# Optimization experiments

Measured on AMD Instinct MI355X. Metric: run time of the kernel, lower is better.

## Reference

```python
import jax, jax.numpy as jnp
import numpy as np

V, D, B, NEG = 100000, 128, 4096, 5
D_INNER = int(D * 2.0 * 2 / 3)  # nGPT FF inner dim = 170

def l2norm(t, axis=-1):
    return t / jnp.linalg.norm(t, axis=axis, keepdims=True)

def setup_inputs() -> dict:
    key = jax.random.key(0)
    ks = jax.random.split(key, 8)
    return {
        "input_ids": jax.random.randint(ks[0], (B,), 0, V),
        "target_ids": jax.random.randint(ks[1], (B,), 0, V),
        "neg_ids": jax.random.randint(ks[2], (B, NEG), 0, V),
        "W_in": jax.random.normal(ks[3], (V, D), jnp.float32) * (1.0 / np.sqrt(D)),
        "W_out": jax.random.normal(ks[4], (V, D), jnp.float32) * (1.0 / np.sqrt(D)),
        "W_hidden": jax.random.normal(ks[5], (D_INNER, D), jnp.float32) * 0.02,
        "W_gate": jax.random.normal(ks[6], (D_INNER, D), jnp.float32) * 0.02,
        "W_ff_out": jax.random.normal(ks[7], (D, D_INNER), jnp.float32) * 0.02,
        "hidden_scale": jnp.ones((D_INNER,), jnp.float32),
        "gate_scale": jnp.ones((D_INNER,), jnp.float32),
        "logit_scale": jnp.full((V,), D ** -0.5, dtype=jnp.float32),  # Scale param init = s_logit_scale
    }

def reference(input_ids, target_ids, neg_ids, W_in, W_out, W_hidden, W_gate,
              W_ff_out, hidden_scale, gate_scale, logit_scale):
    # skipgram: gather normalized input embeddings
    emb = l2norm(W_in)[input_ids]                                  # (B, D)
    # nGPT FeedForward: silu-gated, weights l2-normalized on input dim
    h = (emb @ l2norm(W_hidden).T) * hidden_scale                  # (B, D_INNER)
    g = (emb @ l2norm(W_gate).T) * gate_scale * jnp.sqrt(jnp.float32(D))
    x = jax.nn.silu(g) * h
    x = x @ l2norm(W_ff_out, axis=0).T                             # (B, D), to_out norm_dim_in=False
    # logits over full vocab, scaled by Scale(): param * (init/scale)
    scale_eff = logit_scale * (1.0 / (D ** -0.5))                  # (V,)
    logits = (x @ l2norm(W_out).T) * scale_eff                     # (B, V)
    # negative-sampling loss: gather positive + sampled negative logits
    pos = jnp.take_along_axis(logits, target_ids[:, None], axis=1)  # (B, 1)
    neg = jnp.take_along_axis(logits, neg_ids, axis=1)              # (B, NEG)
    positive_loss = jax.nn.log_sigmoid(pos).mean()
    negative_loss = jax.nn.log_sigmoid(-neg).mean()
    return -(positive_loss + negative_loss)
```

## Files before the change

kernel.cpp:

```cpp
#include <hip/hip_runtime.h>
#include <math.h>

#define DD    128
#define DI    170
#define DIP   176
#define ND4   32
#define ND4H  16
#define NI4P  44
#define BB    4096
#define NNEG  5
#define ROWS  8
#define NBLK  (BB / ROWS)
#define NTHR  512
#define NTASK (ROWS * (1 + NNEG))
#define XOP   132
#define SQRT_D 11.3137084989847603904f

#define WS_WHT 0
#define WS_WGT (ND4 * DIP * 4)
#define WS_WFT (2 * ND4 * DIP * 4)

#define GLOAD_LDS4(gptr, lptr)                                                  \
    __builtin_amdgcn_global_load_lds(                                           \
        (const __attribute__((address_space(1))) void*)(gptr),                  \
        (__attribute__((address_space(3))) void*)(lptr), 4, 0, 0)

#define BAR_LGKM() asm volatile("s_waitcnt lgkmcnt(0)\n\ts_barrier" ::: "memory")

__device__ __forceinline__ float wave_bcast_sum(float v) {
#pragma unroll
    for (int m = 1; m < 64; m <<= 1) v += __shfl_xor(v, m, 64);
    return v;
}

__global__ __launch_bounds__(256) void prep_kernel(
    const float* __restrict__ W_hidden,
    const float* __restrict__ W_gate,
    const float* __restrict__ W_ff_out,
    const float* __restrict__ hidden_scale,
    const float* __restrict__ gate_scale,
    float* __restrict__ ws,
    float* __restrict__ out)
{
    if (blockIdx.x == 0 && threadIdx.x == 0) out[0] = 0.0f;
    const int wave = threadIdx.x >> 6;
    const int lane = threadIdx.x & 63;
    const int t = blockIdx.x * 4 + wave;
    float* whT = ws + WS_WHT;
    float* wgT = ws + WS_WGT;
    float* wfT = ws + WS_WFT;

    if (t < DI) {
        const int v = t;
        float a = W_ff_out[(long)(2 * lane)     * DI + v];
        float b = W_ff_out[(long)(2 * lane + 1) * DI + v];
        float cf = wave_bcast_sum(a * a + b * b);
        float2 ph = ((const float2*)(W_hidden + (long)v * DD))[lane];
        float2 pg = ((const float2*)(W_gate   + (long)v * DD))[lane];
        float sh = wave_bcast_sum(ph.x * ph.x + ph.y * ph.y);
        float sg = wave_bcast_sum(pg.x * pg.x + pg.y * pg.y);
        const float whs = rsqrtf(sh) * hidden_scale[v] * rsqrtf(cf);
        const float wgs = rsqrtf(sg) * gate_scale[v] * SQRT_D;
        const int d4   = lane >> 1;
        const int half = lane & 1;
        float2* dh = (float2*)(whT + ((long)d4 * DIP + v) * 4 + half * 2);
        *dh = make_float2(ph.x * whs, ph.y * whs);
        float2* dg = (float2*)(wgT + ((long)d4 * DIP + v) * 4 + half * 2);
        *dg = make_float2(pg.x * wgs, pg.y * wgs);
    } else if (t < DI + NI4P) {
        const int i4 = t - DI;
#pragma unroll
        for (int rr = 0; rr < 2; ++rr) {
            const int dd = rr * 64 + lane;
            float4 v4;
            if (i4 < 42) {
                float2 lo = *(const float2*)(W_ff_out + (long)dd * DI + 4 * i4);
                float2 hi = *(const float2*)(W_ff_out + (long)dd * DI + 4 * i4 + 2);
                v4 = make_float4(lo.x, lo.y, hi.x, hi.y);
            } else if (i4 == 42) {
                float2 lo = *(const float2*)(W_ff_out + (long)dd * DI + 168);
                v4 = make_float4(lo.x, lo.y, 0.0f, 0.0f);
            } else {
                v4 = make_float4(0.0f, 0.0f, 0.0f, 0.0f);
            }
            *(float4*)(wfT + ((long)i4 * DD + dd) * 4) = v4;
        }
    } else if (t == DI + NI4P || t == DI + NI4P + 1) {
        float* base = (t == DI + NI4P) ? whT : wgT;
        for (int idx = lane; idx < ND4 * 6; idx += 64) {
            const int d4 = idx / 6, c = idx % 6;
            *(float4*)(base + ((long)d4 * DIP + DI + c) * 4) =
                make_float4(0.0f, 0.0f, 0.0f, 0.0f);
        }
    }
}

__global__ __launch_bounds__(NTHR, 4) void main_kernel(
    const int*   __restrict__ input_ids,
    const int*   __restrict__ target_ids,
    const int*   __restrict__ neg_ids,
    const float* __restrict__ W_in,
    const float* __restrict__ W_out,
    const float* __restrict__ logit_scale,
    const float* __restrict__ ws,
    float* __restrict__ out)
{
    __shared__ __align__(16) float s_emb[ROWS][DD];
    __shared__ __align__(16) float s_x[ROWS][DIP];
    __shared__ __align__(16) float s_pp[4][ROWS][DD];
    __shared__ __align__(16) float s_xout[ROWS][XOP];
    __shared__ __align__(16) float s_wout[NTASK][DD];
    __shared__ float s_part[DIP][2 * ROWS + 1];
    __shared__ float s_dp[NTASK][9];
    __shared__ float s_sp[NTASK][9];
    __shared__ float s_psc[NTASK];
    __shared__ float s_ls[NTASK];

    const int tid  = threadIdx.x;
    const int wave = tid >> 6;
    const int lane = tid & 63;
    const int b0   = blockIdx.x * ROWS;

    const float4* whT4 = (const float4*)(ws + WS_WHT);
    const float4* wgT4 = (const float4*)(ws + WS_WGT);
    const float4* wfT4 = (const float4*)(ws + WS_WFT);

    {
        const int id = input_ids[b0 + wave];
        float2 p = ((const float2*)(W_in + (long)id * DD))[lane];
        float s  = wave_bcast_sum(p.x * p.x + p.y * p.y);
        float inv = rsqrtf(s);
        s_emb[wave][2 * lane]     = p.x * inv;
        s_emb[wave][2 * lane + 1] = p.y * inv;
    }
    BAR_LGKM();

    const bool gA = (tid < DIP);
    const bool gB = (tid >= 256 && tid < 256 + DIP);
    const int i = gA ? tid : (gB ? tid - 256 : -1);
    float ah[ROWS], ag[ROWS];
#pragma unroll
    for (int r = 0; r < ROWS; ++r) { ah[r] = 0.0f; ag[r] = 0.0f; }

    if (i >= 0) {
        const int d4lo = gA ? 0 : ND4H;
#pragma unroll 4
        for (int k = 0; k < ND4H; ++k) {
            const int d4 = d4lo + k;
            float4 h4 = whT4[d4 * DIP + i];
            float4 g4 = wgT4[d4 * DIP + i];
#pragma unroll
            for (int r = 0; r < ROWS; ++r) {
                float4 e4 = ((const float4*)s_emb[r])[d4];
                ah[r] += e4.x * h4.x + e4.y * h4.y + e4.z * h4.z + e4.w * h4.w;
                ag[r] += e4.x * g4.x + e4.y * g4.y + e4.z * g4.z + e4.w * g4.w;
            }
        }
    } else if (wave == 3 || wave == 7) {
        const int tb = (wave == 3) ? 0 : 24;
        int   myid  = 0;
        float mypsc = 0.0f;
        if (lane < 24) {
            const int t  = tb + lane;
            const int r  = t / (1 + NNEG);
            const int jj = t % (1 + NNEG);
            const int bidx = b0 + r;
            myid  = (jj == 0) ? target_ids[bidx] : neg_ids[bidx * NNEG + jj - 1];
            mypsc = logit_scale[myid];
        }
#pragma unroll
        for (int k = 0; k < 24; ++k) {
            const int t   = tb + k;
            const int idt = __shfl(myid, k, 64);
            const float* gsrc = W_out + (long)idt * DD;
            GLOAD_LDS4(gsrc + lane,      &s_wout[t][0]);
            GLOAD_LDS4(gsrc + 64 + lane, &s_wout[t][64]);
        }
        if (lane < 24) s_psc[tb + lane] = mypsc;
    }
    if (gB) {
#pragma unroll
        for (int r = 0; r < ROWS; ++r) {
            s_part[i][r]        = ah[r];
            s_part[i][ROWS + r] = ag[r];
        }
    }
    BAR_LGKM();

    if (gA) {
#pragma unroll
        for (int r = 0; r < ROWS; ++r) {
            float h = ah[r] + s_part[i][r];
            float g = ag[r] + s_part[i][ROWS + r];
            float x = (g / (1.0f + __expf(-g))) * h;
            s_x[r][i] = x;
        }
    }
    BAR_LGKM();

    {
        const int dd = tid & 127;
        const int q  = tid >> 7;
        const int i4lo = q * 11;
        float acc[ROWS];
#pragma unroll
        for (int r = 0; r < ROWS; ++r) acc[r] = 0.0f;
#pragma unroll 4
        for (int k = 0; k < 11; ++k) {
            const int i4 = i4lo + k;
            float4 w4 = wfT4[i4 * DD + dd];
#pragma unroll
            for (int r = 0; r < ROWS; ++r) {
                float4 x4 = ((const float4*)s_x[r])[i4];
                acc[r] += w4.x * x4.x + w4.y * x4.y + w4.z * x4.z + w4.w * x4.w;
            }
        }
#pragma unroll
        for (int r = 0; r < ROWS; ++r) s_pp[q][r][dd] = acc[r];
    }
    BAR_LGKM();

    {
        const int dd = tid & 127;
        const int r0 = tid >> 7;
#pragma unroll
        for (int rr = 0; rr < 2; ++rr) {
            const int r = r0 + 4 * rr;
            float v = ((s_pp[0][r][dd] + s_pp[1][r][dd])
                       + s_pp[2][r][dd]) + s_pp[3][r][dd];
            s_xout[r][dd] = v;
        }
    }
    __syncthreads();

    if (tid < NTASK * 8) {
        const int t  = tid >> 3;
        const int c  = tid & 7;
        const int r  = t / (1 + NNEG);
        const float4* wrow4 = (const float4*)&s_wout[t][0];
        const float4* xr4   = (const float4*)&s_xout[r][0];
        float dot = 0.0f, ss = 0.0f;
#pragma unroll
        for (int k2 = 0; k2 < 4; ++k2) {
            const int j = c + 8 * k2;
            float4 w4 = wrow4[j];
            float4 x4 = xr4[j];
            dot += w4.x * x4.x + w4.y * x4.y + w4.z * x4.z + w4.w * x4.w;
            ss  += w4.x * w4.x + w4.y * w4.y + w4.z * w4.z + w4.w * w4.w;
        }
        s_dp[t][c] = dot;
        s_sp[t][c] = ss;
    }
    __syncthreads();

    if (tid < NTASK) {
        const int t  = tid;
        const int jj = t % (1 + NNEG);
        float dot = s_dp[t][0], ss = s_sp[t][0];
#pragma unroll
        for (int c = 1; c < 8; ++c) { dot += s_dp[t][c]; ss += s_sp[t][c]; }
        const float logit = dot * rsqrtf(ss) * s_psc[t] * SQRT_D;
        const float z  = (jj == 0) ? logit : -logit;
        const float ls = fminf(z, 0.0f) - log1pf(__expf(-fabsf(z)));
        s_ls[t] = (jj == 0) ? ls * (1.0f / BB) : ls * (1.0f / (BB * NNEG));
    }
    __syncthreads();
    if (tid == 0) {
        float tot = 0.0f;
#pragma unroll
        for (int t = 0; t < NTASK; ++t) tot += s_ls[t];
        atomicAdd(out, -tot);
    }
}

extern "C" void kernel_launch(void* const* d_in, const int* in_sizes, int n_in,
                              void* d_out, int out_size, void* d_ws, size_t ws_size,
                              hipStream_t stream) {
    (void)in_sizes; (void)n_in; (void)out_size; (void)ws_size;
    const int*   input_ids    = (const int*)  d_in[0];
    const int*   target_ids   = (const int*)  d_in[1];
    const int*   neg_ids      = (const int*)  d_in[2];
    const float* W_in         = (const float*)d_in[3];
    const float* W_out        = (const float*)d_in[4];
    const float* W_hidden     = (const float*)d_in[5];
    const float* W_gate       = (const float*)d_in[6];
    const float* W_ff_out     = (const float*)d_in[7];
    const float* hidden_scale = (const float*)d_in[8];
    const float* gate_scale   = (const float*)d_in[9];
    const float* logit_scale  = (const float*)d_in[10];
    float* out = (float*)d_out;
    float* ws  = (float*)d_ws;

    prep_kernel<<<54, 256, 0, stream>>>(W_hidden, W_gate, W_ff_out,
                                        hidden_scale, gate_scale, ws, out);
    main_kernel<<<NBLK, NTHR, 0, stream>>>(input_ids, target_ids, neg_ids,
                                           W_in, W_out, logit_scale, ws, out);
}
```

Measured before the change: 148.9 us.

## Double block threads and gather W_out rows directly in the dot phase

```diff
diff --git a/kernel.cpp b/kernel.cpp
--- a/kernel.cpp
+++ b/kernel.cpp
@@ -11,7 +11,7 @@
 #define NNEG  5
 #define ROWS  8
 #define NBLK  (BB / ROWS)
-#define NTHR  512
+#define NTHR  1024
 #define NTASK (ROWS * (1 + NNEG))
 #define XOP   132
 #define SQRT_D 11.3137084989847603904f
@@ -20,12 +20,9 @@
 #define WS_WGT (ND4 * DIP * 4)
 #define WS_WFT (2 * ND4 * DIP * 4)
 
-#define GLOAD_LDS4(gptr, lptr)                                                  \
-    __builtin_amdgcn_global_load_lds(                                           \
-        (const __attribute__((address_space(1))) void*)(gptr),                  \
-        (__attribute__((address_space(3))) void*)(lptr), 4, 0, 0)
-
 #define BAR_LGKM() asm volatile("s_waitcnt lgkmcnt(0)\n\ts_barrier" ::: "memory")
+
+#define DOT4(a, b) ((a).x * (b).x + (a).y * (b).y + (a).z * (b).z + (a).w * (b).w)
 
 __device__ __forceinline__ float wave_bcast_sum(float v) {
 #pragma unroll
@@ -95,7 +92,7 @@
     }
 }
 
-__global__ __launch_bounds__(NTHR, 4) void main_kernel(
+__global__ __launch_bounds__(NTHR, 8) void main_kernel(
     const int*   __restrict__ input_ids,
     const int*   __restrict__ target_ids,
     const int*   __restrict__ neg_ids,
@@ -109,8 +106,7 @@
     __shared__ __align__(16) float s_x[ROWS][DIP];
     __shared__ __align__(16) float s_pp[4][ROWS][DD];
     __shared__ __align__(16) float s_xout[ROWS][XOP];
-    __shared__ __align__(16) float s_wout[NTASK][DD];
-    __shared__ float s_part[DIP][2 * ROWS + 1];
+    __shared__ float s_part[DIP][25];
     __shared__ float s_dp[NTASK][9];
     __shared__ float s_sp[NTASK][9];
     __shared__ float s_psc[NTASK];
@@ -125,7 +121,7 @@
     const float4* wgT4 = (const float4*)(ws + WS_WGT);
     const float4* wfT4 = (const float4*)(ws + WS_WFT);
 
-    {
+    if (wave < ROWS) {
         const int id = input_ids[b0 + wave];
         float2 p = ((const float2*)(W_in + (long)id * DD))[lane];
         float s  = wave_bcast_sum(p.x * p.x + p.y * p.y);
@@ -135,109 +131,86 @@
     }
     BAR_LGKM();
 
-    const bool gA = (tid < DIP);
-    const bool gB = (tid >= 256 && tid < 256 + DIP);
-    const int i = gA ? tid : (gB ? tid - 256 : -1);
-    float ah[ROWS], ag[ROWS];
-#pragma unroll
-    for (int r = 0; r < ROWS; ++r) { ah[r] = 0.0f; ag[r] = 0.0f; }
-
-    if (i >= 0) {
-        const int d4lo = gA ? 0 : ND4H;
+    const int quarter = tid >> 8;
+    const int qi      = tid & 255;
+    float a[ROWS];
+#pragma unroll
+    for (int r = 0; r < ROWS; ++r) a[r] = 0.0f;
+
+    if (qi < DIP) {
+        const float4* wT  = (quarter < 2) ? whT4 : wgT4;
+        const int d4lo    = (quarter & 1) * ND4H;
 #pragma unroll 4
         for (int k = 0; k < ND4H; ++k) {
             const int d4 = d4lo + k;
-            float4 h4 = whT4[d4 * DIP + i];
-            float4 g4 = wgT4[d4 * DIP + i];
+            float4 w4 = wT[d4 * DIP + qi];
 #pragma unroll
             for (int r = 0; r < ROWS; ++r) {
                 float4 e4 = ((const float4*)s_emb[r])[d4];
-                ah[r] += e4.x * h4.x + e4.y * h4.y + e4.z * h4.z + e4.w * h4.w;
-                ag[r] += e4.x * g4.x + e4.y * g4.y + e4.z * g4.z + e4.w * g4.w;
+                a[r] += DOT4(e4, w4);
             }
         }
-    } else if (wave == 3 || wave == 7) {
-        const int tb = (wave == 3) ? 0 : 24;
-        int   myid  = 0;
-        float mypsc = 0.0f;
-        if (lane < 24) {
-            const int t  = tb + lane;
-            const int r  = t / (1 + NNEG);
-            const int jj = t % (1 + NNEG);
-            const int bidx = b0 + r;
-            myid  = (jj == 0) ? target_ids[bidx] : neg_ids[bidx * NNEG + jj - 1];
-            mypsc = logit_scale[myid];
-        }
-#pragma unroll
-        for (int k = 0; k < 24; ++k) {
-            const int t   = tb + k;
-            const int idt = __shfl(myid, k, 64);
-            const float* gsrc = W_out + (long)idt * DD;
-            GLOAD_LDS4(gsrc + lane,      &s_wout[t][0]);
-            GLOAD_LDS4(gsrc + 64 + lane, &s_wout[t][64]);
-        }
-        if (lane < 24) s_psc[tb + lane] = mypsc;
-    }
-    if (gB) {
+        if (quarter > 0) {
+#pragma unroll
+            for (int r = 0; r < ROWS; ++r)
+                s_part[qi][(quarter - 1) * ROWS + r] = a[r];
+        }
+    }
+    BAR_LGKM();
+
+    if (quarter == 0 && qi < DIP) {
 #pragma unroll
         for (int r = 0; r < ROWS; ++r) {
-            s_part[i][r]        = ah[r];
-            s_part[i][ROWS + r] = ag[r];
-        }
-    }
-    BAR_LGKM();
-
-    if (gA) {
-#pragma unroll
-        for (int r = 0; r < ROWS; ++r) {
-            float h = ah[r] + s_part[i][r];
-            float g = ag[r] + s_part[i][ROWS + r];
+            float h = a[r] + s_part[qi][r];
+            float g = s_part[qi][ROWS + r] + s_part[qi][2 * ROWS + r];
             float x = (g / (1.0f + __expf(-g))) * h;
-            s_x[r][i] = x;
+            s_x[r][qi] = x;
         }
     }
     BAR_LGKM();
 
     {
         const int dd = tid & 127;
-        const int q  = tid >> 7;
+        const int q  = (tid >> 7) & 3;
+        const int rh = tid >> 9;
         const int i4lo = q * 11;
-        float acc[ROWS];
-#pragma unroll
-        for (int r = 0; r < ROWS; ++r) acc[r] = 0.0f;
+        float acc[4];
+#pragma unroll
+        for (int rr = 0; rr < 4; ++rr) acc[rr] = 0.0f;
 #pragma unroll 4
         for (int k = 0; k < 11; ++k) {
             const int i4 = i4lo + k;
             float4 w4 = wfT4[i4 * DD + dd];
 #pragma unroll
-            for (int r = 0; r < ROWS; ++r) {
+            for (int rr = 0; rr < 4; ++rr) {
+                const int r = rh * 4 + rr;
                 float4 x4 = ((const float4*)s_x[r])[i4];
-                acc[r] += w4.x * x4.x + w4.y * x4.y + w4.z * x4.z + w4.w * x4.w;
+                acc[rr] += w4.x * x4.x + w4.y * x4.y + w4.z * x4.z + w4.w * x4.w;
             }
         }
 #pragma unroll
-        for (int r = 0; r < ROWS; ++r) s_pp[q][r][dd] = acc[r];
+        for (int rr = 0; rr < 4; ++rr) s_pp[q][rh * 4 + rr][dd] = acc[rr];
     }
     BAR_LGKM();
 
     {
         const int dd = tid & 127;
-        const int r0 = tid >> 7;
-#pragma unroll
-        for (int rr = 0; rr < 2; ++rr) {
-            const int r = r0 + 4 * rr;
-            float v = ((s_pp[0][r][dd] + s_pp[1][r][dd])
-                       + s_pp[2][r][dd]) + s_pp[3][r][dd];
-            s_xout[r][dd] = v;
-        }
-    }
-    __syncthreads();
+        const int r  = tid >> 7;
+        float v = ((s_pp[0][r][dd] + s_pp[1][r][dd])
+                   + s_pp[2][r][dd]) + s_pp[3][r][dd];
+        s_xout[r][dd] = v;
+    }
+    BAR_LGKM();
 
     if (tid < NTASK * 8) {
         const int t  = tid >> 3;
         const int c  = tid & 7;
         const int r  = t / (1 + NNEG);
-        const float4* wrow4 = (const float4*)&s_wout[t][0];
+        const int jj = t % (1 + NNEG);
+        const int bidx = b0 + r;
+        const int id = (jj == 0) ? target_ids[bidx] : neg_ids[bidx * NNEG + jj - 1];
+        if (c == 0) s_psc[t] = logit_scale[id];
+        const float4* wrow4 = (const float4*)(W_out + (long)id * DD);
         const float4* xr4   = (const float4*)&s_xout[r][0];
         float dot = 0.0f, ss = 0.0f;
 #pragma unroll
@@ -251,7 +224,7 @@
         s_dp[t][c] = dot;
         s_sp[t][c] = ss;
     }
-    __syncthreads();
+    BAR_LGKM();
 
     if (tid < NTASK) {
         const int t  = tid;
@@ -264,7 +237,7 @@
         const float ls = fminf(z, 0.0f) - log1pf(__expf(-fabsf(z)));
         s_ls[t] = (jj == 0) ? ls * (1.0f / BB) : ls * (1.0f / (BB * NNEG));
     }
-    __syncthreads();
+    BAR_LGKM();
     if (tid == 0) {
         float tot = 0.0f;
 #pragma unroll
```

Result: no change. 151.7 us (+1.9%).
